# Optimization experiments

Measured on AMD Instinct MI355X. Metric: run time of the kernel, lower is better.

## Reference

```python
import jax, jax.numpy as jnp
import numpy as np

B, K, DIM = 8192, 256, 1024


def setup_inputs() -> dict:
    key = jax.random.key(0)
    k1, k2, k3 = jax.random.split(key, 3)
    x = jax.random.normal(k1, (B, DIM), dtype=jnp.float32)
    centers = jax.random.uniform(k2, (K, DIM), dtype=jnp.float32)
    # torch init: D = 0.2 * rand + 0.9
    D = 0.2 * jax.random.uniform(k3, (K, DIM), dtype=jnp.float32) + 0.9
    return {"x": x, "centers": centers, "D": D}


def reference(x, centers, D):
    # Per-class axis-aligned (diagonal) covariance
    D_abs = jnp.abs(D) + 1e-4                      # [K, DIM]
    D_inv = 1.0 / D_abs                            # [K, DIM]
    log_det = jnp.sum(jnp.log(D_abs), axis=1)      # [K]
    det_scale_factor = -0.5 * log_det
    det_scale_safe = jnp.exp(det_scale_factor - jnp.max(det_scale_factor))  # [K]

    # dist_sq[b,k] = sum_d (x[b,d]-c[k,d])^2 * D_inv[k,d]
    # Expanded quadratic form avoids materializing the [B,K,DIM] diff tensor.
    x2 = jnp.einsum('bd,kd->bk', x * x, D_inv)             # [B, K]
    xc = jnp.einsum('bd,kd->bk', x, centers * D_inv)       # [B, K]
    c2 = jnp.sum(centers * centers * D_inv, axis=1)        # [K]
    dist_sq = x2 - 2.0 * xc + c2[None, :]                  # [B, K]

    # Gaussian path (isCauchy=False)
    expo = -0.5 * dist_sq
    expo_safe = expo - jnp.max(expo, axis=-1, keepdims=True)
    numer_safe = det_scale_safe[None, :] * jnp.exp(expo_safe)
    denom_safe = jnp.sum(numer_safe, axis=1, keepdims=True)
    resp = numer_safe / denom_safe                         # [B, K]
    return resp
```

## Files before the change

### kernel.cpp

```cpp
#include <hip/hip_runtime.h>

typedef _Float16 f16x8 __attribute__((ext_vector_type(8)));
typedef _Float16 f16x4 __attribute__((ext_vector_type(4)));
typedef float f32x4 __attribute__((ext_vector_type(4)));

#define B_N 8192
#define K_N 256
#define DIM_N 1024

__global__ __launch_bounds__(256) void prep_w(const float* __restrict__ Dm,
                                              const float* __restrict__ Cm,
                                              _Float16* __restrict__ Upk,
                                              _Float16* __restrict__ Wpk,
                                              float* __restrict__ ec) {
    const int k = blockIdx.x, t = threadIdx.x;
    const int d = t * 4;
    const float4 dv = *(const float4*)(Dm + (size_t)k * DIM_N + d);
    const float4 cv = *(const float4*)(Cm + (size_t)k * DIM_N + d);
    float dd[4] = {dv.x, dv.y, dv.z, dv.w};
    float cc[4] = {cv.x, cv.y, cv.z, cv.w};
    f16x4 uo, wo;
    float llog = 0.f, lc2 = 0.f;
#pragma unroll
    for (int i = 0; i < 4; ++i) {
        float da = fabsf(dd[i]) + 1e-4f;
        float dinv = 1.0f / da;
        llog += logf(da);
        lc2 += cc[i] * cc[i] * dinv;
        uo[i] = (_Float16)(dinv - 1.0f);
        wo[i] = (_Float16)(-2.0f * cc[i] * dinv);
    }
    const int cg = k >> 4, cl = k & 15;
    const int kc = d >> 5, g = (d >> 3) & 3, j0 = d & 7;
    const size_t off = ((size_t)(cg * 32 + kc) * 64 + g * 16 + cl) * 8 + j0;
    *(f16x4*)(Upk + off) = uo;
    *(f16x4*)(Wpk + off) = wo;
    float both = llog + lc2;
#pragma unroll
    for (int m = 1; m <= 32; m <<= 1) both += __shfl_xor(both, m, 64);
    __shared__ float sb[4];
    if ((t & 63) == 0) sb[t >> 6] = both;
    __syncthreads();
    if (t == 0) ec[k] = -0.5f * (sb[0] + sb[1] + sb[2] + sb[3]);
}

__global__ __launch_bounds__(512, 1)
void gmm_gemm(const float* __restrict__ x,
              const _Float16* __restrict__ Upk,
              const _Float16* __restrict__ Wpk,
              float* __restrict__ S) {
    __shared__ __align__(16) char xlds[65536];

    const int tid = threadIdx.x;
    const int wave = tid >> 6, lane = tid & 63;
    const int l15 = lane & 15, g4 = lane >> 4;
    const int wr = wave >> 2, wc = wave & 3;
    const int bid = blockIdx.x;
    const int rowp = bid & 127, colp = bid >> 7;
    const int bRow = rowp * 64, bCol = colp * 128;

    const int sr = tid >> 3, q4 = tid & 7;
    const float* xq = x + (size_t)(bRow + sr) * DIM_N + q4 * 4;
    int wAddr[8];
#pragma unroll
    for (int j = 0; j < 8; ++j) {
        const int cl = j >> 1, k2 = j & 1;
        const int fi = (sr >> 4) * 2 + k2;
        wAddr[j] = cl * 8192 + fi * 1024 + ((sr & 15) + 16 * (q4 >> 1)) * 16 + (q4 & 1) * 8;
    }

    const _Float16* upb = Upk + (size_t)(colp * 8 + wc * 2) * 32 * 512 + lane * 8;
    const _Float16* wpb = Wpk + (size_t)(colp * 8 + wc * 2) * 32 * 512 + lane * 8;

    f32x4 acc[2][2];
#pragma unroll
    for (int m = 0; m < 2; ++m)
#pragma unroll
        for (int n = 0; n < 2; ++n) { f32x4 z = {0.f, 0.f, 0.f, 0.f}; acc[m][n] = z; }

    float4 xs[2][8];
    f16x8 ub[2][2][2], wb[2][2][2];

    auto issueQ = [&](int bank, int q) {
#pragma unroll
        for (int j = 0; j < 8; ++j) xs[bank][j] = *(const float4*)(xq + q * 256 + j * 32);
    };
    auto writeQ = [&](int bank, int buf) {
        char* base = xlds + buf * 32768;
#pragma unroll
        for (int j = 0; j < 8; ++j) {
            const float4 v = xs[bank][j];
            f16x4 h = {(_Float16)v.x, (_Float16)v.y, (_Float16)v.z, (_Float16)v.w};
            *(f16x4*)(base + wAddr[j]) = h;
        }
    };
    auto issueB = [&](int bank, int c) {
#pragma unroll
        for (int n = 0; n < 2; ++n)
#pragma unroll
            for (int k2 = 0; k2 < 2; ++k2) {
                const int kc = c * 2 + k2;
                ub[bank][n][k2] = *(const f16x8*)(upb + (size_t)(n * 32 + kc) * 512);
                wb[bank][n][k2] = *(const f16x8*)(wpb + (size_t)(n * 32 + kc) * 512);
            }
    };
    auto compute = [&](int c, int bank) {
        const char* base = xlds + ((c >> 2) & 1) * 32768 + (c & 3) * 8192;
        f16x8 axf[2][2];
#pragma unroll
        for (int m = 0; m < 2; ++m)
#pragma unroll
            for (int k2 = 0; k2 < 2; ++k2) {
                const int fi = (wr * 2 + m) * 2 + k2;
                axf[m][k2] = *(const f16x8*)(base + fi * 1024 + lane * 16);
            }
#pragma unroll
        for (int m = 0; m < 2; ++m)
#pragma unroll
            for (int k2 = 0; k2 < 2; ++k2) {
                const f16x8 a2 = axf[m][k2] * axf[m][k2];
#pragma unroll
                for (int n = 0; n < 2; ++n) {
                    acc[m][n] = __builtin_amdgcn_mfma_f32_16x16x32_f16(a2, ub[bank][n][k2], acc[m][n], 0, 0, 0);
                    acc[m][n] = __builtin_amdgcn_mfma_f32_16x16x32_f16(axf[m][k2], wb[bank][n][k2], acc[m][n], 0, 0, 0);
                }
            }
    };

    issueB(0, 0); issueB(1, 1);
    issueQ(0, 0); issueQ(1, 1);
    writeQ(0, 0);
    asm volatile("s_waitcnt lgkmcnt(0)" ::: "memory");
    __builtin_amdgcn_s_barrier();
    __builtin_amdgcn_sched_barrier(0);
    writeQ(1, 1);
    issueQ(0, 2);
    compute(0, 0);  issueB(0, 2);
    compute(1, 1);  issueB(1, 3);
    compute(2, 0);  issueB(0, 4);
    compute(3, 1);  issueB(1, 5);
    asm volatile("s_waitcnt lgkmcnt(0)" ::: "memory");
    __builtin_amdgcn_s_barrier();
    __builtin_amdgcn_sched_barrier(0);
    writeQ(0, 0);
    issueQ(1, 3);
    compute(4, 0);  issueB(0, 6);
    compute(5, 1);  issueB(1, 7);
    compute(6, 0);  issueB(0, 8);
    compute(7, 1);  issueB(1, 9);
    asm volatile("s_waitcnt lgkmcnt(0)" ::: "memory");
    __builtin_amdgcn_s_barrier();
    __builtin_amdgcn_sched_barrier(0);
    writeQ(1, 1);
    compute(8, 0);   issueB(0, 10);
    compute(9, 1);   issueB(1, 11);
    compute(10, 0);  issueB(0, 12);
    compute(11, 1);  issueB(1, 13);
    asm volatile("s_waitcnt lgkmcnt(0)" ::: "memory");
    __builtin_amdgcn_s_barrier();
    __builtin_amdgcn_sched_barrier(0);
    compute(12, 0);  issueB(0, 14);
    compute(13, 1);  issueB(1, 15);
    compute(14, 0);
    compute(15, 1);

#pragma unroll
    for (int m = 0; m < 2; ++m) {
        const int rb = bRow + wr * 32 + m * 16 + g4 * 4;
        const int cb = bCol + wc * 32 + l15;
#pragma unroll
        for (int j = 0; j < 4; ++j) {
            float* p = S + (size_t)(rb + j) * K_N + cb;
            p[0] = acc[m][0][j];
            p[16] = acc[m][1][j];
        }
    }
}

__global__ __launch_bounds__(256)
void gmm_soft(float* __restrict__ S, const float* __restrict__ ecg) {
    const int tid = threadIdx.x;
    const int wave = tid >> 6, lane = tid & 63;
    const int r = blockIdx.x * 4 + wave;
    const int k0 = lane * 4;
    float4 s = *(const float4*)(S + (size_t)r * K_N + k0);
    float4 cv = *(const float4*)(ecg + k0);
    float e[4] = {fmaf(-0.5f, s.x, cv.x), fmaf(-0.5f, s.y, cv.y),
                  fmaf(-0.5f, s.z, cv.z), fmaf(-0.5f, s.w, cv.w)};
    float m = fmaxf(fmaxf(e[0], e[1]), fmaxf(e[2], e[3]));
#pragma unroll
    for (int msk = 1; msk <= 32; msk <<= 1) m = fmaxf(m, __shfl_xor(m, msk, 64));
    float p[4], sum = 0.f;
#pragma unroll
    for (int j = 0; j < 4; ++j) {
        p[j] = __expf(e[j] - m);
        sum += p[j];
    }
#pragma unroll
    for (int msk = 1; msk <= 32; msk <<= 1) sum += __shfl_xor(sum, msk, 64);
    const float inv = 1.0f / sum;
    *(float4*)(S + (size_t)r * K_N + k0) = make_float4(p[0] * inv, p[1] * inv, p[2] * inv, p[3] * inv);
}

extern "C" void kernel_launch(void* const* d_in, const int* in_sizes, int n_in,
                              void* d_out, int out_size, void* d_ws, size_t ws_size,
                              hipStream_t stream) {
    const float* x = (const float*)d_in[0];
    const float* cen = (const float*)d_in[1];
    const float* Dm = (const float*)d_in[2];
    float* out = (float*)d_out;

    char* ws = (char*)d_ws;
    _Float16* Upk = (_Float16*)(ws);
    _Float16* Wpk = (_Float16*)(ws + 524288);
    float* ec = (float*)(ws + 1048576);

    prep_w<<<dim3(K_N), dim3(256), 0, stream>>>(Dm, cen, Upk, Wpk, ec);
    gmm_gemm<<<dim3(256), dim3(512), 0, stream>>>(x, Upk, Wpk, out);
    gmm_soft<<<dim3(B_N / 4), dim3(256), 0, stream>>>(out, ec);
}
```

Measured before the change: 32.65 us.

## Halve GEMM block tile, swizzle full x tile in LDS, prioritize MFMA

Changes the GEMM from 512-thread blocks with 64x128 tiles to 256-thread blocks with 32x128 tiles, launching twice as many blocks with two per CU allowed. The x tile is stored whole in LDS in a row-major XOR-swizzled layout, so no buffer is reused and reads avoid bank conflicts. x loads are issued earlier and s_setprio raises wave priority around the MFMA sequence. The aim is better latency hiding through more independent blocks, at the cost of halving reuse of the U/W fragments per block.

```diff
diff --git a/kernel.cpp b/kernel.cpp
--- a/kernel.cpp
+++ b/kernel.cpp
@@ -44,7 +44,7 @@
     if (t == 0) ec[k] = -0.5f * (sb[0] + sb[1] + sb[2] + sb[3]);
 }
 
-__global__ __launch_bounds__(512, 1)
+__global__ __launch_bounds__(256, 2)
 void gmm_gemm(const float* __restrict__ x,
               const _Float16* __restrict__ Upk,
               const _Float16* __restrict__ Wpk,
@@ -54,23 +54,21 @@
     const int tid = threadIdx.x;
     const int wave = tid >> 6, lane = tid & 63;
     const int l15 = lane & 15, g4 = lane >> 4;
-    const int wr = wave >> 2, wc = wave & 3;
     const int bid = blockIdx.x;
-    const int rowp = bid & 127, colp = bid >> 7;
-    const int bRow = rowp * 64, bCol = colp * 128;
-
-    const int sr = tid >> 3, q4 = tid & 7;
-    const float* xq = x + (size_t)(bRow + sr) * DIM_N + q4 * 4;
-    int wAddr[8];
+    const int rowp = bid >> 1, colp = bid & 1;
+    const int bRow = rowp * 32, bCol = colp * 128;
+
+    const int srow = tid >> 3, sd = (tid & 7) * 4;
+    const float* xq = x + (size_t)(bRow + srow) * DIM_N + sd;
+    int wB[8];
 #pragma unroll
     for (int j = 0; j < 8; ++j) {
-        const int cl = j >> 1, k2 = j & 1;
-        const int fi = (sr >> 4) * 2 + k2;
-        wAddr[j] = cl * 8192 + fi * 1024 + ((sr & 15) + 16 * (q4 >> 1)) * 16 + (q4 & 1) * 8;
-    }
-
-    const _Float16* upb = Upk + (size_t)(colp * 8 + wc * 2) * 32 * 512 + lane * 8;
-    const _Float16* wpb = Wpk + (size_t)(colp * 8 + wc * 2) * 32 * 512 + lane * 8;
+        const int slot = (sd >> 3) + 4 * j;
+        wB[j] = srow * 512 + (((slot ^ (srow & 7)) << 4) | ((sd & 4) << 1));
+    }
+
+    const _Float16* upb = Upk + (size_t)(colp * 8 + wave * 2) * 32 * 512 + lane * 8;
+    const _Float16* wpb = Wpk + (size_t)(colp * 8 + wave * 2) * 32 * 512 + lane * 8;
 
     f32x4 acc[2][2];
 #pragma unroll
@@ -78,20 +76,20 @@
 #pragma unroll
         for (int n = 0; n < 2; ++n) { f32x4 z = {0.f, 0.f, 0.f, 0.f}; acc[m][n] = z; }
 
-    float4 xs[2][8];
-    f16x8 ub[2][2][2], wb[2][2][2];
+    float4 xr[2][8];
+    f16x8 ub2[2][2][2], wb2[2][2][2];
 
     auto issueQ = [&](int bank, int q) {
 #pragma unroll
-        for (int j = 0; j < 8; ++j) xs[bank][j] = *(const float4*)(xq + q * 256 + j * 32);
-    };
-    auto writeQ = [&](int bank, int buf) {
-        char* base = xlds + buf * 32768;
+        for (int j = 0; j < 8; ++j) xr[bank][j] = *(const float4*)(xq + q * 256 + j * 32);
+    };
+    auto writeQ = [&](int bank, int q) {
+        char* base = xlds + q * 16384;
 #pragma unroll
         for (int j = 0; j < 8; ++j) {
-            const float4 v = xs[bank][j];
+            const float4 v = xr[bank][j];
             f16x4 h = {(_Float16)v.x, (_Float16)v.y, (_Float16)v.z, (_Float16)v.w};
-            *(f16x4*)(base + wAddr[j]) = h;
+            *(f16x4*)(base + wB[j]) = h;
         }
     };
     auto issueB = [&](int bank, int c) {
@@ -100,20 +98,23 @@
 #pragma unroll
             for (int k2 = 0; k2 < 2; ++k2) {
                 const int kc = c * 2 + k2;
-                ub[bank][n][k2] = *(const f16x8*)(upb + (size_t)(n * 32 + kc) * 512);
-                wb[bank][n][k2] = *(const f16x8*)(wpb + (size_t)(n * 32 + kc) * 512);
+                ub2[bank][n][k2] = *(const f16x8*)(upb + (size_t)(n * 32 + kc) * 512);
+                wb2[bank][n][k2] = *(const f16x8*)(wpb + (size_t)(n * 32 + kc) * 512);
             }
     };
     auto compute = [&](int c, int bank) {
-        const char* base = xlds + ((c >> 2) & 1) * 32768 + (c & 3) * 8192;
+        const char* base = xlds + (c >> 2) * 16384;
+        const int cl = c & 3;
         f16x8 axf[2][2];
 #pragma unroll
         for (int m = 0; m < 2; ++m)
 #pragma unroll
             for (int k2 = 0; k2 < 2; ++k2) {
-                const int fi = (wr * 2 + m) * 2 + k2;
-                axf[m][k2] = *(const f16x8*)(base + fi * 1024 + lane * 16);
+                const int row = m * 16 + l15;
+                const int slot = cl * 8 + k2 * 4 + g4;
+                axf[m][k2] = *(const f16x8*)(base + row * 512 + ((slot ^ (l15 & 7)) << 4));
             }
+        __builtin_amdgcn_s_setprio(1);
 #pragma unroll
         for (int m = 0; m < 2; ++m)
 #pragma unroll
@@ -121,53 +122,54 @@
                 const f16x8 a2 = axf[m][k2] * axf[m][k2];
 #pragma unroll
                 for (int n = 0; n < 2; ++n) {
-                    acc[m][n] = __builtin_amdgcn_mfma_f32_16x16x32_f16(a2, ub[bank][n][k2], acc[m][n], 0, 0, 0);
-                    acc[m][n] = __builtin_amdgcn_mfma_f32_16x16x32_f16(axf[m][k2], wb[bank][n][k2], acc[m][n], 0, 0, 0);
+                    acc[m][n] = __builtin_amdgcn_mfma_f32_16x16x32_f16(a2, ub2[bank][n][k2], acc[m][n], 0, 0, 0);
+                    acc[m][n] = __builtin_amdgcn_mfma_f32_16x16x32_f16(axf[m][k2], wb2[bank][n][k2], acc[m][n], 0, 0, 0);
                 }
             }
+        __builtin_amdgcn_s_setprio(0);
     };
 
     issueB(0, 0); issueB(1, 1);
     issueQ(0, 0); issueQ(1, 1);
     writeQ(0, 0);
+    issueQ(0, 2);
     asm volatile("s_waitcnt lgkmcnt(0)" ::: "memory");
     __builtin_amdgcn_s_barrier();
     __builtin_amdgcn_sched_barrier(0);
     writeQ(1, 1);
-    issueQ(0, 2);
-    compute(0, 0);  issueB(0, 2);
-    compute(1, 1);  issueB(1, 3);
-    compute(2, 0);  issueB(0, 4);
-    compute(3, 1);  issueB(1, 5);
-    asm volatile("s_waitcnt lgkmcnt(0)" ::: "memory");
-    __builtin_amdgcn_s_barrier();
-    __builtin_amdgcn_sched_barrier(0);
-    writeQ(0, 0);
     issueQ(1, 3);
-    compute(4, 0);  issueB(0, 6);
-    compute(5, 1);  issueB(1, 7);
-    compute(6, 0);  issueB(0, 8);
-    compute(7, 1);  issueB(1, 9);
-    asm volatile("s_waitcnt lgkmcnt(0)" ::: "memory");
-    __builtin_amdgcn_s_barrier();
-    __builtin_amdgcn_sched_barrier(0);
-    writeQ(1, 1);
-    compute(8, 0);   issueB(0, 10);
-    compute(9, 1);   issueB(1, 11);
-    compute(10, 0);  issueB(0, 12);
-    compute(11, 1);  issueB(1, 13);
-    asm volatile("s_waitcnt lgkmcnt(0)" ::: "memory");
-    __builtin_amdgcn_s_barrier();
-    __builtin_amdgcn_sched_barrier(0);
-    compute(12, 0);  issueB(0, 14);
-    compute(13, 1);  issueB(1, 15);
+    compute(0, 0); issueB(0, 2);
+    compute(1, 1); issueB(1, 3);
+    compute(2, 0); issueB(0, 4);
+    compute(3, 1); issueB(1, 5);
+    asm volatile("s_waitcnt lgkmcnt(0)" ::: "memory");
+    __builtin_amdgcn_s_barrier();
+    __builtin_amdgcn_sched_barrier(0);
+    writeQ(0, 2);
+    compute(4, 0); issueB(0, 6);
+    compute(5, 1); issueB(1, 7);
+    compute(6, 0); issueB(0, 8);
+    compute(7, 1); issueB(1, 9);
+    asm volatile("s_waitcnt lgkmcnt(0)" ::: "memory");
+    __builtin_amdgcn_s_barrier();
+    __builtin_amdgcn_sched_barrier(0);
+    writeQ(1, 3);
+    compute(8, 0);  issueB(0, 10);
+    compute(9, 1);  issueB(1, 11);
+    compute(10, 0); issueB(0, 12);
+    compute(11, 1); issueB(1, 13);
+    asm volatile("s_waitcnt lgkmcnt(0)" ::: "memory");
+    __builtin_amdgcn_s_barrier();
+    __builtin_amdgcn_sched_barrier(0);
+    compute(12, 0); issueB(0, 14);
+    compute(13, 1); issueB(1, 15);
     compute(14, 0);
     compute(15, 1);
 
 #pragma unroll
     for (int m = 0; m < 2; ++m) {
-        const int rb = bRow + wr * 32 + m * 16 + g4 * 4;
-        const int cb = bCol + wc * 32 + l15;
+        const int rb = bRow + m * 16 + g4 * 4;
+        const int cb = bCol + wave * 32 + l15;
 #pragma unroll
         for (int j = 0; j < 4; ++j) {
             float* p = S + (size_t)(rb + j) * K_N + cb;
@@ -216,6 +218,6 @@
     float* ec = (float*)(ws + 1048576);
 
     prep_w<<<dim3(K_N), dim3(256), 0, stream>>>(Dm, cen, Upk, Wpk, ec);
-    gmm_gemm<<<dim3(256), dim3(512), 0, stream>>>(x, Upk, Wpk, out);
+    gmm_gemm<<<dim3(512), dim3(256), 0, stream>>>(x, Upk, Wpk, out);
     gmm_soft<<<dim3(B_N / 4), dim3(256), 0, stream>>>(out, ec);
 }
```

Measured after the change: 36.77 us. 12.6% more time.
